# Kernel tuning notes

Measured on AMD Instinct MI355X. Metric: run time of the kernel, lower is better.

Reference implementation:

```python
import jax, jax.numpy as jnp
import numpy as np

RATE = 0.1
RANDOM_PORTION = 0.1


def setup_inputs() -> dict:
    key = jax.random.key(0)
    x = jax.random.normal(key, (32, 524288), dtype=jnp.float32)
    return {"x": x}


def reference(x) -> jnp.ndarray:
    # Training-mode forward of RandomTopKModifier.
    b = x.shape[0]
    xf = x.reshape(b, -1)                      # [B, N]
    n = xf.shape[1]
    k = max(1, round(RATE * n))

    # 1) top-k by magnitude (indices only; unsorted is fine, set-equivalent)
    _, topk_idx = jax.lax.top_k(jnp.abs(xf), k)            # [B, k] int32

    # 2) build per-element sampling probabilities:
    #    random_portion mass spread over the N-k non-topk slots,
    #    (1 - random_portion) mass spread over the k topk slots.
    rows = jnp.arange(b)[:, None]                           # [B, 1]
    probs = jnp.full_like(xf, RANDOM_PORTION / (n - k))
    probs = probs.at[rows, topk_idx].set((1.0 - RANDOM_PORTION) / k)

    # 3) weighted sampling of k indices WITHOUT replacement
    #    (torch.multinomial(probs, k)) via the Gumbel-top-k trick.
    g = jax.random.gumbel(jax.random.key(42), xf.shape, dtype=xf.dtype)
    _, sel_idx = jax.lax.top_k(jnp.log(probs) + g, k)       # [B, k]

    # 4) scatter a binary mask and apply it
    mask = jnp.zeros_like(xf).at[rows, sel_idx].set(1.0)
    return (mask * xf).reshape(x.shape)
```

## Files before the change

### kernel.cpp

```cpp
#include <hip/hip_runtime.h>
#include <stdint.h>


static constexpr uint32_t BB = 32;
static constexpr uint32_t NN = 524288;
static constexpr uint32_t KK = 52429;
static constexpr uint32_t W = 64;
static constexpr uint32_t CHUNK = NN / W;
static constexpr uint32_t SEGCAP1 = 1024;
static constexpr uint32_t CAP1 = W * SEGCAP1;
static constexpr uint32_t SEGCAP2 = 1280;
static constexpr uint32_t CAP2 = W * SEGCAP2;
static constexpr uint32_t SELCAP = 512;
static constexpr uint32_t SENT = 0xFFFFFFFFu;
static constexpr uint32_t T1KEY = 0x3FD00000u;
static constexpr uint32_t LO1 = T1KEY;
static constexpr uint32_t LO2 = 0x3EC4CCCCu;

__device__ __forceinline__ float xla_logf(float xin) {
#pragma clang fp contract(off)
  float x = fmaxf(xin, __uint_as_float(0x00800000u));
  uint32_t bits = __float_as_uint(x);
  float e = (float)((int)(bits >> 23) - 126);
  x = __uint_as_float((bits & 0x807fffffu) | 0x3f000000u);
  bool mlt = x < 0.707106781186547524f;
  float tmp = mlt ? x : 0.0f;
  x = x - 1.0f;
  e = e - (mlt ? 1.0f : 0.0f);
  x = x + tmp;
  float x2 = x * x;
  float x3 = x2 * x;
  float y, y1, y2;
  y  = 7.0376836292E-2f * x + -1.1514610310E-1f;
  y1 = -1.2420140846E-1f * x + 1.4249322787E-1f;
  y2 = 2.0000714765E-1f * x + -2.4999993993E-1f;
  y  = y * x + 1.1676998740E-1f;
  y1 = y1 * x + -1.6668057665E-1f;
  y2 = y2 * x + 3.3333331174E-1f;
  y  = y * x3 + y1;
  y  = y * x3 + y2;
  y  = y * x3;
  y1 = e * -2.12194440e-4f;
  tmp = x2 * 0.5f;
  y = y + y1;
  x = x - tmp;
  y2 = e * 0.693359375f;
  x = x + y;
  x = x + y2;
  return x;
}

__device__ __forceinline__ float c_top_val()  { return xla_logf((float)((1.0 - 0.1) / 52429.0)); }
__device__ __forceinline__ float c_rand_val() { return xla_logf((float)(0.1 / 471859.0)); }

__device__ __forceinline__ uint32_t tf_bits(uint32_t i) {
  const uint32_t ks0 = 0u, ks1 = 42u, ks2 = 0x1BD11BDAu ^ 42u;
  uint32_t x0 = 0u + ks0;
  uint32_t x1 = i + ks1;
#define TFR(r) { x0 += x1; x1 = (x1 << (r)) | (x1 >> (32 - (r))); x1 ^= x0; }
  TFR(13) TFR(15) TFR(26) TFR(6)
  x0 += ks1; x1 += ks2 + 1u;
  TFR(17) TFR(29) TFR(16) TFR(24)
  x0 += ks2; x1 += ks0 + 2u;
  TFR(13) TFR(15) TFR(26) TFR(6)
  x0 += ks0; x1 += ks1 + 3u;
  TFR(17) TFR(29) TFR(16) TFR(24)
  x0 += ks1; x1 += ks2 + 4u;
  TFR(13) TFR(15) TFR(26) TFR(6)
  x0 += ks2; x1 += ks0 + 5u;
#undef TFR
  return x0 ^ x1;
}

__device__ __forceinline__ uint32_t key_x(float v) { return __float_as_uint(v) & 0x7fffffffu; }
__device__ __forceinline__ uint32_t key_s(float v) {
  uint32_t b = __float_as_uint(v);
  return (b & 0x80000000u) ? ~b : (b | 0x80000000u);
}


__global__ void __launch_bounds__(256)
k_candcoll1(const float* __restrict__ src,
            uint32_t* __restrict__ cidx, uint32_t* __restrict__ ckey) {
  __shared__ uint32_t lcnt;
  uint32_t row = blockIdx.y, seg = blockIdx.x;
  if (threadIdx.x == 0) lcnt = 0u;
  __syncthreads();
  uint32_t lane = threadIdx.x & 63u;
  uint32_t colbase = seg * CHUNK;
  uint32_t base = row * CAP1 + seg * SEGCAP1;
  const float4* p = (const float4*)(src + (size_t)row * NN + colbase);
  for (uint32_t j = threadIdx.x; j < CHUNK / 4; j += 256) {
    float4 v = p[j];
    float vv[4] = {v.x, v.y, v.z, v.w};
#pragma unroll
    for (int e = 0; e < 4; ++e) {
      uint32_t key = key_x(vv[e]);
      bool cand = (key >= T1KEY);
      unsigned long long bal = __ballot(cand);
      if (bal) {
        uint32_t leader = (uint32_t)__ffsll((long long)bal) - 1u;
        uint32_t bw = 0;
        if (lane == leader) bw = atomicAdd(&lcnt, (uint32_t)__popcll(bal));
        bw = __shfl(bw, (int)leader);
        if (cand) {
          uint32_t li = bw + (uint32_t)__popcll(bal & ((1ull << lane) - 1ull));
          if (li < SEGCAP1) { cidx[base + li] = colbase + j * 4 + e; ckey[base + li] = key; }
        }
      }
    }
  }
  __syncthreads();
  uint32_t c = (lcnt < SEGCAP1) ? lcnt : SEGCAP1;
  for (uint32_t j = c + threadIdx.x; j < SEGCAP1; j += 256) ckey[base + j] = SENT;
}

__device__ __forceinline__ void scan_hist(const uint32_t* lh, uint32_t* csA,
                                          uint32_t* sh, uint32_t kk, uint32_t t) {
  uint32_t s0 = 0;
  if (t < 256) {
#pragma unroll
    for (int j = 0; j < 8; ++j) s0 += lh[t * 8 + j];
    csA[t] = s0;
  }
  __syncthreads();
#pragma unroll
  for (uint32_t stp = 1; stp < 256; stp <<= 1) {
    uint32_t v = 0;
    if (t < 256 && t + stp < 256) v = csA[t + stp];
    __syncthreads();
    if (t < 256) csA[t] += v;
    __syncthreads();
  }
  if (t < 256) {
    uint32_t Sst = csA[t] - s0;
    if (Sst < kk && Sst + s0 >= kk) {
      uint32_t acc = Sst, bin = t * 8;
      for (int b2 = (int)t * 8 + 7; b2 >= (int)t * 8; --b2) {
        uint32_t hv = lh[b2];
        if (acc + hv >= kk) { bin = (uint32_t)b2; break; }
        acc += hv;
      }
      sh[0] = bin; sh[1] = kk - acc;
    }
  }
  __syncthreads();
}

__global__ void __launch_bounds__(1024)
k_select(const uint32_t* __restrict__ cidx, const uint32_t* __restrict__ ckey,
         uint32_t cap, uint32_t LO, uint32_t* __restrict__ st, uint32_t* __restrict__ sel) {
  __shared__ uint32_t lh[2048];
  __shared__ uint32_t csA[256];
  __shared__ uint32_t lkey[1024];
  __shared__ uint32_t lidx[1024];
  __shared__ uint32_t sh[8];
  uint32_t row = blockIdx.x;
  uint32_t t = threadIdx.x;
  const uint4* pk = (const uint4*)(ckey + (size_t)row * cap);
  for (uint32_t b = t; b < 2048; b += 1024) lh[b] = 0u;
  __syncthreads();
  for (uint32_t j0 = 0; j0 < cap / 4; j0 += 4 * 1024) {
    uint4 k4[4];
#pragma unroll
    for (int u = 0; u < 4; ++u) k4[u] = pk[j0 + u * 1024 + t];
#pragma unroll
    for (int u = 0; u < 4; ++u) {
      uint32_t kk[4] = {k4[u].x, k4[u].y, k4[u].z, k4[u].w};
#pragma unroll
      for (int e = 0; e < 4; ++e) {
        if (kk[e] != SENT) {
          uint32_t bin = (kk[e] - LO) >> 13;
          if (bin > 2047u) bin = 2047u;
          atomicAdd(&lh[bin], 1u);
        }
      }
    }
  }
  __syncthreads();
  scan_hist(lh, csA, sh, KK, t);
  uint32_t bstar = sh[0], kkW = sh[1];
  if (t == 0) sh[4] = 0u;
  __syncthreads();
  for (uint32_t j0 = 0; j0 < cap / 4; j0 += 4 * 1024) {
    uint4 k4[4];
#pragma unroll
    for (int u = 0; u < 4; ++u) k4[u] = pk[j0 + u * 1024 + t];
#pragma unroll
    for (int u = 0; u < 4; ++u) {
      uint32_t kk[4] = {k4[u].x, k4[u].y, k4[u].z, k4[u].w};
#pragma unroll
      for (int e = 0; e < 4; ++e) {
        if (kk[e] != SENT && ((kk[e] - LO) >> 13) == bstar) {
          uint32_t li = atomicAdd(&sh[4], 1u);
          if (li < 1024) { lkey[li] = kk[e]; lidx[li] = cidx[(size_t)row * cap + (j0 + u * 1024 + t) * 4 + e]; }
        }
      }
    }
  }
  __syncthreads();
  uint32_t cnt = sh[4]; if (cnt > 1024) cnt = 1024;
  if (t < cnt) {
    uint32_t myk = lkey[t], myi = lidx[t];
    uint32_t gt = 0, eq = 0, eqlt = 0;
    for (uint32_t b = 0; b < cnt; ++b) {
      uint32_t kb = lkey[b];
      gt += (kb > myk) ? 1u : 0u;
      if (kb == myk) { eq++; eqlt += (lidx[b] < myi) ? 1u : 0u; }
    }
    if (gt < kkW && gt + eq >= kkW) {
      uint32_t m = kkW - gt;
      if (eqlt == 0) { st[row * 8 + 2] = myk; st[row * 8 + 4] = (m > SELCAP) ? SELCAP : m; }
      if (eqlt < m && eqlt < SELCAP) sel[row * SELCAP + eqlt] = myi;
    }
  }
}

__global__ void __launch_bounds__(256)
k_compute_u(const float* __restrict__ x, const uint32_t* __restrict__ st1,
            const uint32_t* __restrict__ sel1,
            uint32_t* __restrict__ cidx, uint32_t* __restrict__ ckey) {
  __shared__ uint32_t lcnt;
  uint32_t row = blockIdx.y, seg = blockIdx.x;
  if (threadIdx.x == 0) lcnt = 0u;
  __syncthreads();
  const uint32_t BT = (uint32_t)ceilf(0.150f  * 8388608.0f) << 9;
  const uint32_t BR = (uint32_t)ceilf(0.9765f * 8388608.0f) << 9;
  uint32_t lane = threadIdx.x & 63u;
  uint32_t thr1 = st1[row * 8 + 2];
  uint32_t m1 = st1[row * 8 + 4];
  uint32_t colbase = seg * CHUNK;
  uint32_t base = row * CAP2 + seg * SEGCAP2;
  uint32_t ibase = (row << 19) + colbase;
  const float4* px = (const float4*)(x + (size_t)row * NN + colbase);
  for (uint32_t j = threadIdx.x; j < CHUNK / 4; j += 256) {
    float4 v = px[j];
    float vv[4] = {v.x, v.y, v.z, v.w};
#pragma unroll
    for (int e = 0; e < 4; ++e) {
      uint32_t col = colbase + j * 4 + e;
      uint32_t key = key_x(vv[e]);
      bool istop = key > thr1;
      if (key == thr1) {
        for (uint32_t q = 0; q < m1; ++q)
          if (sel1[row * SELCAP + q] == col) { istop = true; break; }
      }
      uint32_t b = tf_bits(ibase + j * 4 + e);
      bool cand = (b >= (istop ? BT : BR));
      unsigned long long bal = __ballot(cand);
      if (bal) {
        uint32_t leader = (uint32_t)__ffsll((long long)bal) - 1u;
        uint32_t bw = 0;
        if (lane == leader) bw = atomicAdd(&lcnt, (uint32_t)__popcll(bal));
        bw = __shfl(bw, (int)leader);
        if (cand) {
          uint32_t li = bw + (uint32_t)__popcll(bal & ((1ull << lane) - 1ull));
          if (li < SEGCAP2) {
            cidx[base + li] = col | (istop ? 0x80000000u : 0u);
            ckey[base + li] = b;
          }
        }
      }
    }
  }
  __syncthreads();
  uint32_t c = (lcnt < SEGCAP2) ? lcnt : SEGCAP2;
  for (uint32_t j = c + threadIdx.x; j < SEGCAP2; j += 256) {
    cidx[base + j] = SENT;
    ckey[base + j] = SENT;
  }
}

__global__ void __launch_bounds__(256)
k_finish(uint32_t* __restrict__ cidx, uint32_t* __restrict__ ckey) {
  uint32_t row = blockIdx.y, seg = blockIdx.x;
  uint32_t base = row * CAP2 + seg * SEGCAP2;
  float CT = c_top_val(), CR = c_rand_val();
  for (uint32_t j = threadIdx.x; j < SEGCAP2; j += 256) {
    uint32_t ci = cidx[base + j];
    if (ci == SENT) continue;
    uint32_t b = ckey[base + j];
    float u = __uint_as_float((b >> 9) | 0x3f800000u) - 1.0f;
    u = fmaxf(u, 1.17549435e-38f);
    float nl = -xla_logf(u);
    float g = -xla_logf(nl);
    float s = ((ci >> 31) ? CT : CR) + g;
    ckey[base + j] = key_s(s);
    cidx[base + j] = ci & 0x7FFFFFFFu;
  }
}

__global__ void __launch_bounds__(256)
k_scatter(const float* __restrict__ x, float* __restrict__ out,
          const uint32_t* __restrict__ cidx, const uint32_t* __restrict__ ckey,
          const uint32_t* __restrict__ st2, const uint32_t* __restrict__ sel2) {
  uint32_t row = blockIdx.y, seg = blockIdx.x;
  uint32_t thr2 = st2[row * 8 + 2];
  uint32_t m2 = st2[row * 8 + 4];
  uint32_t base = row * CAP2 + seg * SEGCAP2;
  for (uint32_t j = threadIdx.x; j < SEGCAP2; j += 256) {
    uint32_t key = ckey[base + j];
    if (key == SENT) continue;
    uint32_t col = cidx[base + j];
    bool take = key > thr2;
    if (key == thr2) {
      for (uint32_t q = 0; q < m2; ++q)
        if (sel2[row * SELCAP + q] == col) { take = true; break; }
    }
    if (take) out[(size_t)row * NN + col] = x[(size_t)row * NN + col];
  }
}

extern "C" void kernel_launch(void* const* d_in, const int* in_sizes, int n_in,
                              void* d_out, int out_size, void* d_ws, size_t ws_size,
                              hipStream_t stream) {
  const float* x = (const float*)d_in[0];
  float* out = (float*)d_out;

  uint32_t* w = (uint32_t*)d_ws;
  uint32_t* st1   = w;
  uint32_t* st2   = st1 + BB * 8;
  uint32_t* sel1  = st2 + BB * 8;
  uint32_t* sel2  = sel1 + BB * SELCAP;
  uint32_t* cidx  = sel2 + BB * SELCAP;
  uint32_t* ckey  = cidx + BB * CAP2;

  dim3 blk(256), blkS(1024), gridF(W, BB), gridR(BB);

  k_candcoll1<<<gridF, blk, 0, stream>>>(x, cidx, ckey);
  k_select<<<gridR, blkS, 0, stream>>>(cidx, ckey, CAP1, LO1, st1, sel1);

  k_compute_u<<<gridF, blk, 0, stream>>>(x, st1, sel1, cidx, ckey);

  k_finish<<<gridF, blk, 0, stream>>>(cidx, ckey);

  k_select<<<gridR, blkS, 0, stream>>>(cidx, ckey, CAP2, LO2, st2, sel2);

  hipMemsetAsync(out, 0, (size_t)BB * NN * 4u, stream);
  k_scatter<<<gridF, blk, 0, stream>>>(x, out, cidx, ckey, st2, sel2);
}
```

Measured before the change: 155.0 us.

## Build top-k bitmask from candidates instead of rereading input in compute_u

A new k_mask kernel marks the first-stage top-k members in a per-row bitmask, built from the compacted candidate list and the tie selections. k_compute_u then reads that bitmask instead of rereading the full input x and scanning the tie list per element, which cuts its global read traffic. The wave-level ballot aggregation of atomics is replaced by a per-element shared atomicAdd in both collection kernels, and the hash loop is unrolled by four. This adds a memset and an extra kernel launch, and per-element atomics may contend more heavily.

```diff
diff --git a/kernel.cpp b/kernel.cpp
--- a/kernel.cpp
+++ b/kernel.cpp
@@ -16,6 +16,7 @@
 static constexpr uint32_t T1KEY = 0x3FD00000u;
 static constexpr uint32_t LO1 = T1KEY;
 static constexpr uint32_t LO2 = 0x3EC4CCCCu;
+static constexpr uint32_t MASKW = NN / 32;
 
 __device__ __forceinline__ float xla_logf(float xin) {
 #pragma clang fp contract(off)
@@ -86,7 +87,6 @@
   uint32_t row = blockIdx.y, seg = blockIdx.x;
   if (threadIdx.x == 0) lcnt = 0u;
   __syncthreads();
-  uint32_t lane = threadIdx.x & 63u;
   uint32_t colbase = seg * CHUNK;
   uint32_t base = row * CAP1 + seg * SEGCAP1;
   const float4* p = (const float4*)(src + (size_t)row * NN + colbase);
@@ -96,17 +96,9 @@
 #pragma unroll
     for (int e = 0; e < 4; ++e) {
       uint32_t key = key_x(vv[e]);
-      bool cand = (key >= T1KEY);
-      unsigned long long bal = __ballot(cand);
-      if (bal) {
-        uint32_t leader = (uint32_t)__ffsll((long long)bal) - 1u;
-        uint32_t bw = 0;
-        if (lane == leader) bw = atomicAdd(&lcnt, (uint32_t)__popcll(bal));
-        bw = __shfl(bw, (int)leader);
-        if (cand) {
-          uint32_t li = bw + (uint32_t)__popcll(bal & ((1ull << lane) - 1ull));
-          if (li < SEGCAP1) { cidx[base + li] = colbase + j * 4 + e; ckey[base + li] = key; }
-        }
+      if (key >= T1KEY) {
+        uint32_t li = atomicAdd(&lcnt, 1u);
+        if (li < SEGCAP1) { cidx[base + li] = colbase + j * 4 + e; ckey[base + li] = key; }
       }
     }
   }
@@ -217,48 +209,61 @@
 }
 
 __global__ void __launch_bounds__(256)
-k_compute_u(const float* __restrict__ x, const uint32_t* __restrict__ st1,
-            const uint32_t* __restrict__ sel1,
+k_mask(const uint32_t* __restrict__ cidx, const uint32_t* __restrict__ ckey,
+       const uint32_t* __restrict__ st1, const uint32_t* __restrict__ sel1,
+       uint32_t* __restrict__ mask) {
+  uint32_t row = blockIdx.y, part = blockIdx.x;
+  uint32_t thr1 = st1[row * 8 + 2];
+  uint32_t* mrow = mask + row * MASKW;
+  uint32_t base = row * CAP1 + part * (CAP1 / 8);
+  for (uint32_t j = threadIdx.x; j < CAP1 / 8; j += 256) {
+    uint32_t key = ckey[base + j];
+    if (key != SENT && key > thr1) {
+      uint32_t col = cidx[base + j];
+      atomicOr(&mrow[col >> 5], 1u << (col & 31u));
+    }
+  }
+  if (part == 0) {
+    uint32_t m1 = st1[row * 8 + 4];
+    for (uint32_t q = threadIdx.x; q < m1; q += 256) {
+      uint32_t col = sel1[row * SELCAP + q];
+      atomicOr(&mrow[col >> 5], 1u << (col & 31u));
+    }
+  }
+}
+
+__global__ void __launch_bounds__(256)
+k_compute_u(const uint32_t* __restrict__ mask,
             uint32_t* __restrict__ cidx, uint32_t* __restrict__ ckey) {
   __shared__ uint32_t lcnt;
   uint32_t row = blockIdx.y, seg = blockIdx.x;
   if (threadIdx.x == 0) lcnt = 0u;
   __syncthreads();
-  const uint32_t BT = (uint32_t)ceilf(0.150f  * 8388608.0f) << 9;
-  const uint32_t BR = (uint32_t)ceilf(0.9765f * 8388608.0f) << 9;
-  uint32_t lane = threadIdx.x & 63u;
-  uint32_t thr1 = st1[row * 8 + 2];
-  uint32_t m1 = st1[row * 8 + 4];
+  const uint32_t BT = (uint32_t)(0.150f  * 8388608.0f + 0.999999f) << 9;
+  const uint32_t BR = (uint32_t)(0.9765f * 8388608.0f + 0.999999f) << 9;
   uint32_t colbase = seg * CHUNK;
   uint32_t base = row * CAP2 + seg * SEGCAP2;
   uint32_t ibase = (row << 19) + colbase;
-  const float4* px = (const float4*)(x + (size_t)row * NN + colbase);
-  for (uint32_t j = threadIdx.x; j < CHUNK / 4; j += 256) {
-    float4 v = px[j];
-    float vv[4] = {v.x, v.y, v.z, v.w};
-#pragma unroll
-    for (int e = 0; e < 4; ++e) {
-      uint32_t col = colbase + j * 4 + e;
-      uint32_t key = key_x(vv[e]);
-      bool istop = key > thr1;
-      if (key == thr1) {
-        for (uint32_t q = 0; q < m1; ++q)
-          if (sel1[row * SELCAP + q] == col) { istop = true; break; }
-      }
-      uint32_t b = tf_bits(ibase + j * 4 + e);
-      bool cand = (b >= (istop ? BT : BR));
-      unsigned long long bal = __ballot(cand);
-      if (bal) {
-        uint32_t leader = (uint32_t)__ffsll((long long)bal) - 1u;
-        uint32_t bw = 0;
-        if (lane == leader) bw = atomicAdd(&lcnt, (uint32_t)__popcll(bal));
-        bw = __shfl(bw, (int)leader);
-        if (cand) {
-          uint32_t li = bw + (uint32_t)__popcll(bal & ((1ull << lane) - 1ull));
-          if (li < SEGCAP2) {
-            cidx[base + li] = col | (istop ? 0x80000000u : 0u);
-            ckey[base + li] = b;
-          }
+  const uint32_t* mrow = mask + row * MASKW;
+#pragma unroll 1
+  for (uint32_t j = threadIdx.x; j < CHUNK; j += 1024) {
+    uint32_t jj[4] = {j, j + 256, j + 512, j + 768};
+    uint32_t bb[4], mw[4];
+#pragma unroll
+    for (int u = 0; u < 4; ++u) {
+      bb[u] = tf_bits(ibase + jj[u]);
+      mw[u] = mrow[(colbase + jj[u]) >> 5];
+    }
+#pragma unroll
+    for (int u = 0; u < 4; ++u) {
+      uint32_t col = colbase + jj[u];
+      bool istop = (mw[u] >> (col & 31u)) & 1u;
+      bool cand = bb[u] >= (istop ? BT : BR);
+      if (cand) {
+        uint32_t li = atomicAdd(&lcnt, 1u);
+        if (li < SEGCAP2) {
+          cidx[base + li] = col | (istop ? 0x80000000u : 0u);
+          ckey[base + li] = bb[u];
         }
       }
     }
@@ -322,15 +327,19 @@
   uint32_t* st2   = st1 + BB * 8;
   uint32_t* sel1  = st2 + BB * 8;
   uint32_t* sel2  = sel1 + BB * SELCAP;
-  uint32_t* cidx  = sel2 + BB * SELCAP;
+  uint32_t* mask  = sel2 + BB * SELCAP;
+  uint32_t* cidx  = mask + BB * MASKW;
   uint32_t* ckey  = cidx + BB * CAP2;
 
-  dim3 blk(256), blkS(1024), gridF(W, BB), gridR(BB);
+  dim3 blk(256), blkS(1024), gridF(W, BB), gridR(BB), gridM(8, BB);
 
   k_candcoll1<<<gridF, blk, 0, stream>>>(x, cidx, ckey);
   k_select<<<gridR, blkS, 0, stream>>>(cidx, ckey, CAP1, LO1, st1, sel1);
 
-  k_compute_u<<<gridF, blk, 0, stream>>>(x, st1, sel1, cidx, ckey);
+  hipMemsetAsync(mask, 0, (size_t)BB * MASKW * 4u, stream);
+  k_mask<<<gridM, blk, 0, stream>>>(cidx, ckey, st1, sel1, mask);
+
+  k_compute_u<<<gridF, blk, 0, stream>>>(mask, cidx, ckey);
 
   k_finish<<<gridF, blk, 0, stream>>>(cidx, ckey);
 
```

After: 200.9 us. +29.7%, slower.
